# Kernel tuning notes

Hardware: AMD Instinct MI355X
Metric: run time of the kernel (lower is better)

The kernel has to match this reference:

```python
import jax, jax.numpy as jnp
import numpy as np

N_ENT = 50000
N_REL2 = 100   # num_relations * 2
N_BASES = 16
DIM = 64
N_EDGES = 100000


def _rgcn_conv(x, edge_index, edge_type, edge_norm, basis, att, root, bias):
    # x: [N, D]; basis: [B, D, D]; att: [R, B]; root: [D, D]; bias: [D]
    src = edge_index[0]
    dst = edge_index[1]
    num_nodes = x.shape[0]
    # Per-edge relation weight is w[edge_type] with w = att @ basis (reshaped).
    # By linearity we contract x_j with each basis first, then mix with the
    # per-edge attention coefficients -- same math, avoids the [E, D, D] gather.
    coeff = att[edge_type]                          # [E, B]
    xb = jnp.einsum('ei,bio->ebo', x[src], basis)   # [E, B, D]
    msg = jnp.einsum('eb,ebo->eo', coeff, xb)       # [E, D]
    msg = msg * edge_norm[:, None]
    # scatter-mean aggregation at target nodes
    s = jax.ops.segment_sum(msg, dst, num_segments=num_nodes)
    cnt = jax.ops.segment_sum(jnp.ones((msg.shape[0],), msg.dtype), dst,
                              num_segments=num_nodes)
    agg = s / jnp.maximum(cnt, 1.0)[:, None]
    # root transform + bias
    return agg + x @ root + bias


def setup_inputs() -> dict:
    key = jax.random.key(0)
    ks = jax.random.split(key, 12)
    E = N_EDGES
    inp = {
        'entity': jnp.arange(N_ENT, dtype=jnp.int64) if jax.config.jax_enable_x64 else jnp.arange(N_ENT, dtype=jnp.int32),
        'edge_index': jax.random.randint(ks[0], (2, E), 0, N_ENT),
        'edge_type': jax.random.randint(ks[1], (E,), 0, N_REL2),
        'edge_norm': jax.random.uniform(ks[2], (E,), dtype=jnp.float32),
        'emb': jax.random.normal(ks[3], (N_ENT, DIM), dtype=jnp.float32) * 0.1,
        'basis1': jax.random.normal(ks[4], (N_BASES, DIM, DIM), dtype=jnp.float32) * 0.05,
        'att1': jax.random.normal(ks[5], (N_REL2, N_BASES), dtype=jnp.float32) * 0.1,
        'root1': jax.random.normal(ks[6], (DIM, DIM), dtype=jnp.float32) * 0.05,
        'bias1': jnp.zeros((DIM,), dtype=jnp.float32),
        'basis2': jax.random.normal(ks[7], (N_BASES, DIM, DIM), dtype=jnp.float32) * 0.05,
        'att2': jax.random.normal(ks[8], (N_REL2, N_BASES), dtype=jnp.float32) * 0.1,
        'root2': jax.random.normal(ks[9], (DIM, DIM), dtype=jnp.float32) * 0.05,
        'bias2': jnp.zeros((DIM,), dtype=jnp.float32),
    }
    return inp


def reference(entity, edge_index, edge_type, edge_norm, emb,
              basis1, att1, root1, bias1, basis2, att2, root2, bias2):
    x = emb[entity]                                  # embedding lookup [N, D]
    x = _rgcn_conv(x, edge_index, edge_type, edge_norm, basis1, att1, root1, bias1)
    x = _rgcn_conv(x, edge_index, edge_type, edge_norm, basis2, att2, root2, bias2)
    return x
```

## Files before the change

kernel.cpp:

```cpp
#include <hip/hip_runtime.h>

#define NN 50000
#define NR 100
#define NB 16
#define D  64
#define NE 100000
#define NE2 (NE + 16 * NR)

#define HB  196
#define EPB 512
#define ZB  196
#define GB  ((NN * 16 + 255) / 256)

#define GROUPS 2
#define EPBK (64 * GROUPS)
#define EGRID ((NE2 + EPBK - 1) / EPBK)

#define NPBK 128
#define NGRID ((NN + NPBK - 1) / NPBK)

typedef float f32x4  __attribute__((ext_vector_type(4)));
typedef short bf16x8 __attribute__((ext_vector_type(8)));
typedef unsigned short u16;

__device__ __forceinline__ short f2bf(float f) {
    unsigned u = __float_as_uint(f);
    return (short)((u + 0x7FFFu + ((u >> 16) & 1u)) >> 16);
}

__device__ __forceinline__ float bf2f(u16 u) {
    return __uint_as_float((unsigned)u << 16);
}

__device__ __forceinline__ bf16x8 pack8(f32x4 a, f32x4 b) {
    bf16x8 t;
    t[0] = f2bf(a.x); t[1] = f2bf(a.y); t[2] = f2bf(a.z); t[3] = f2bf(a.w);
    t[4] = f2bf(b.x); t[5] = f2bf(b.y); t[6] = f2bf(b.z); t[7] = f2bf(b.w);
    return t;
}

__global__ __launch_bounds__(256) void prep_all(
    const float* __restrict__ att1, const float* __restrict__ basis1,
    const float* __restrict__ root1,
    const float* __restrict__ att2, const float* __restrict__ basis2,
    const float* __restrict__ root2,
    const int* __restrict__ entity, const f32x4* __restrict__ emb4,
    float* __restrict__ Wt1, float* __restrict__ Wt2,
    float* __restrict__ rT1, float* __restrict__ rT2,
    f32x4* __restrict__ x04, int* __restrict__ deg, int* __restrict__ nodeCur)
{
    __shared__ float t[64 * 65];
    int b = blockIdx.x;
    if (b < 2 * NR) {
        int layer = b >= NR;
        int r = layer ? b - NR : b;
        const float* att   = layer ? att2 : att1;
        const float* basis = layer ? basis2 : basis1;
        float*       Wt    = layer ? Wt2 : Wt1;
        float a[NB];
#pragma unroll
        for (int bb = 0; bb < NB; ++bb) a[bb] = att[r * NB + bb];
#pragma unroll
        for (int i = 0; i < 16; ++i) {
            int idx = i * 256 + threadIdx.x;
            float acc = 0.f;
#pragma unroll
            for (int bb = 0; bb < NB; ++bb) acc += a[bb] * basis[bb * 4096 + idx];
            t[(idx >> 6) * 65 + (idx & 63)] = acc;
        }
        __syncthreads();
#pragma unroll
        for (int i = 0; i < 16; ++i) {
            int j = i * 256 + threadIdx.x;
            Wt[(size_t)r * 4096 + j] = t[(j & 63) * 65 + (j >> 6)];
        }
    } else if (b < 2 * NR + 2) {
        const float* root = (b == 2 * NR) ? root1 : root2;
        float*       rT   = (b == 2 * NR) ? rT1 : rT2;
#pragma unroll
        for (int i = 0; i < 16; ++i) {
            int idx = i * 256 + threadIdx.x;
            t[(idx >> 6) * 65 + (idx & 63)] = root[idx];
        }
        __syncthreads();
#pragma unroll
        for (int i = 0; i < 16; ++i) {
            int j = i * 256 + threadIdx.x;
            rT[j] = t[(j & 63) * 65 + (j >> 6)];
        }
    } else if (b < 2 * NR + 2 + ZB) {
        int i = (b - (2 * NR + 2)) * 256 + threadIdx.x;
        deg[i] = 0; nodeCur[i] = 0;
    } else {
        int idx = (b - (2 * NR + 2 + ZB)) * 256 + threadIdx.x;
        if (idx < NN * 16) {
            int n = idx >> 4;
            int q = idx & 15;
            x04[idx] = emb4[(size_t)entity[n] * 16 + q];
        }
    }
}

__global__ __launch_bounds__(256) void hist_edges(
    const int* __restrict__ et, const int* __restrict__ dst,
    int* __restrict__ blockHist, int* __restrict__ deg)
{
    __shared__ int lh[NR];
    for (int i = threadIdx.x; i < NR; i += 256) lh[i] = 0;
    __syncthreads();
#pragma unroll
    for (int i = 0; i < EPB / 256; ++i) {
        int e = blockIdx.x * EPB + i * 256 + threadIdx.x;
        if (e < NE) {
            atomicAdd(&lh[et[e]], 1);
            atomicAdd(&deg[dst[e]], 1);
        }
    }
    __syncthreads();
    for (int i = threadIdx.x; i < NR; i += 256)
        blockHist[blockIdx.x * NR + i] = lh[i];
}

__global__ __launch_bounds__(256) void scans(
    const int* __restrict__ blockHist, int* __restrict__ blockPrefix,
    int* __restrict__ relTot, const int* __restrict__ deg,
    int* __restrict__ nodePre, int* __restrict__ blockSumN)
{
    __shared__ int sc[256];
    int t = threadIdx.x;
    if (blockIdx.x < NR) {
        int r = blockIdx.x;
        int v = (t < HB) ? blockHist[t * NR + r] : 0;
        sc[t] = v;
        __syncthreads();
#pragma unroll
        for (int off = 1; off < 256; off <<= 1) {
            int a = (t >= off) ? sc[t - off] : 0;
            __syncthreads();
            sc[t] += a;
            __syncthreads();
        }
        if (t < HB) blockPrefix[t * NR + r] = sc[t] - v;
        if (t == 0) relTot[r] = sc[255];
    } else {
        int b = blockIdx.x - NR;
        int n = b * 256 + t;
        int v = deg[n];
        sc[t] = v;
        __syncthreads();
#pragma unroll
        for (int off = 1; off < 256; off <<= 1) {
            int a = (t >= off) ? sc[t - off] : 0;
            __syncthreads();
            sc[t] += a;
            __syncthreads();
        }
        nodePre[n] = sc[t] - v;
        if (t == 255) blockSumN[b] = sc[255];
    }
}

__global__ __launch_bounds__(256) void scanK(
    const int* __restrict__ relTot, const int* __restrict__ blockSumN,
    int* __restrict__ offs, int* __restrict__ nbG, int* __restrict__ nodeBB,
    int* __restrict__ srcS, float* __restrict__ normS, int* __restrict__ rS)
{
    __shared__ int totL[NR];
    __shared__ int offL[NR + 1];
    __shared__ int sc2[256];
    int t = threadIdx.x;
    if (t < NR) totL[t] = relTot[t];
    int v2 = (t < ZB) ? blockSumN[t] : 0;
    sc2[t] = v2;
    __syncthreads();
    if (t == 0) {
        int off = 0;
        for (int r = 0; r < NR; ++r) {
            offL[r] = off;
            off = (off + totL[r] + 15) & ~15;
        }
        offL[NR] = off;
    }
    __syncthreads();
#pragma unroll
    for (int off = 1; off < 256; off <<= 1) {
        int a = (t >= off) ? sc2[t - off] : 0;
        __syncthreads();
        sc2[t] += a;
        __syncthreads();
    }
    if (t < ZB) nodeBB[t] = sc2[t] - v2;
    if (t == 0) nodeBB[ZB] = sc2[255];
    if (t <= NR) offs[t] = offL[t];
    if (t == 0) nbG[0] = offL[NR];
    if (t < NR) {
        int g0 = offL[t] + totL[t], g1 = offL[t + 1];
        for (int p = g0; p < g1; ++p) { srcS[p] = 0; normS[p] = 0.f; rS[p] = t; }
    }
}

__global__ __launch_bounds__(256) void scatter2(
    const int* __restrict__ src, const int* __restrict__ dst,
    const int* __restrict__ et, const float* __restrict__ en,
    const int* __restrict__ offs, const int* __restrict__ blockPrefix,
    const int* __restrict__ nodePre, const int* __restrict__ nodeBlockBase,
    int* __restrict__ nodeCur, int* __restrict__ srcS,
    float* __restrict__ normS, int* __restrict__ rS, int* __restrict__ dstIdx)
{
    __shared__ int lcur[NR];
    for (int i = threadIdx.x; i < NR; i += 256)
        lcur[i] = offs[i] + blockPrefix[blockIdx.x * NR + i];
    __syncthreads();
#pragma unroll
    for (int i = 0; i < EPB / 256; ++i) {
        int e = blockIdx.x * EPB + i * 256 + threadIdx.x;
        if (e < NE) {
            int r = et[e];
            int p = atomicAdd(&lcur[r], 1);
            srcS[p] = src[e]; normS[p] = en[e]; rS[p] = r;
            int n = dst[e];
            int q = nodeBlockBase[n >> 8] + nodePre[n] + atomicAdd(&nodeCur[n], 1);
            dstIdx[q] = p;
        }
    }
}

__global__ __launch_bounds__(256) void edge_mfma(
    const int* __restrict__ srcS, const float* __restrict__ normS,
    const int* __restrict__ rS, const int* __restrict__ nbG,
    const float* __restrict__ x, const float* __restrict__ Wt,
    u16* __restrict__ msg)
{
    int tid = threadIdx.x;
    int lane = tid & 63, wid = tid >> 6;
    int c15 = lane & 15, kg = lane >> 4;
    int padTot = nbG[0];
    int rcur = -1;
    bf16x8 B[4][2];

#pragma unroll 1
    for (int g = 0; g < GROUPS; ++g) {
        int gs = blockIdx.x * EPBK + wid * (16 * GROUPS) + g * 16;
        if (gs >= padTot) break;
        int r = __builtin_amdgcn_readfirstlane(rS[gs]);
        if (r != rcur) {
            rcur = r;
            const float* __restrict__ Wr = Wt + (size_t)r * 4096;
#pragma unroll
            for (int nt = 0; nt < 4; ++nt)
#pragma unroll
                for (int ks = 0; ks < 2; ++ks) {
                    const f32x4* p = (const f32x4*)(Wr + (nt * 16 + c15) * 64 + ks * 32 + kg * 8);
                    B[nt][ks] = pack8(p[0], p[1]);
                }
        }
        int e  = gs + c15;
        float nrm = normS[e];
        int   sn  = srcS[e];
        const f32x4* xr  = (const f32x4*)(x + (size_t)sn * 64 + kg * 8);
        const f32x4* xr2 = (const f32x4*)(x + (size_t)sn * 64 + 32 + kg * 8);
        bf16x8 A0 = pack8(xr[0]  * nrm, xr[1]  * nrm);
        bf16x8 A1 = pack8(xr2[0] * nrm, xr2[1] * nrm);

        f32x4 z = {0.f, 0.f, 0.f, 0.f};
        f32x4 acc[4] = {z, z, z, z};
#pragma unroll
        for (int nt = 0; nt < 4; ++nt) {
            acc[nt] = __builtin_amdgcn_mfma_f32_16x16x32_bf16(A0, B[nt][0], acc[nt], 0, 0, 0);
            acc[nt] = __builtin_amdgcn_mfma_f32_16x16x32_bf16(A1, B[nt][1], acc[nt], 0, 0, 0);
        }
#pragma unroll
        for (int nt = 0; nt < 4; ++nt)
#pragma unroll
            for (int j = 0; j < 4; ++j)
                msg[(size_t)(gs + kg * 4 + j) * 64 + nt * 16 + c15] =
                    (u16)f2bf(acc[nt][j]);
    }
}

__global__ __launch_bounds__(256) void agg_mean(
    const u16* __restrict__ msg, const int* __restrict__ dstIdx,
    const int* __restrict__ nodePre, const int* __restrict__ nodeBB,
    float* __restrict__ agg)
{
    int n    = blockIdx.x * 4 + (threadIdx.x >> 6);
    int lane = threadIdx.x & 63;
    if (n >= NN) return;
    int blk  = n >> 8;
    int base = nodeBB[blk];
    int lo = base + nodePre[n];
    int hi = ((n & 255) == 255) ? nodeBB[blk + 1] : base + nodePre[n + 1];
    float acc = 0.f;
    for (int q = lo; q < hi; ++q)
        acc += bf2f(msg[(size_t)dstIdx[q] * 64 + lane]);
    float c = (float)(hi - lo);
    c = c > 1.f ? c : 1.f;
    agg[(size_t)n * 64 + lane] = acc / c;
}

__global__ __launch_bounds__(256) void node_mfma(
    const float* __restrict__ x, const float* __restrict__ agg,
    const float* __restrict__ rT, const float* __restrict__ bias,
    float* __restrict__ out)
{
    int tid = threadIdx.x;
    int lane = tid & 63, wid = tid >> 6;
    int c15 = lane & 15, kg = lane >> 4;

    bf16x8 B[4][2];
#pragma unroll
    for (int nt = 0; nt < 4; ++nt)
#pragma unroll
        for (int ks = 0; ks < 2; ++ks) {
            const f32x4* p = (const f32x4*)(rT + (nt * 16 + c15) * 64 + ks * 32 + kg * 8);
            B[nt][ks] = pack8(p[0], p[1]);
        }
    float bv[4];
#pragma unroll
    for (int nt = 0; nt < 4; ++nt) bv[nt] = bias[nt * 16 + c15];

#pragma unroll 1
    for (int g = 0; g < 2; ++g) {
        int gs = blockIdx.x * NPBK + wid * 32 + g * 16;
        if (gs >= NN) break;
        int ge = gs + 16 < NN ? gs + 16 : NN;

        int n  = gs + c15;
        int nc = n < ge ? n : ge - 1;
        const f32x4* xr  = (const f32x4*)(x + (size_t)nc * 64 + kg * 8);
        const f32x4* xr2 = (const f32x4*)(x + (size_t)nc * 64 + 32 + kg * 8);
        bf16x8 A0 = pack8(xr[0], xr[1]);
        bf16x8 A1 = pack8(xr2[0], xr2[1]);

        f32x4 z = {0.f, 0.f, 0.f, 0.f};
        f32x4 acc[4] = {z, z, z, z};
#pragma unroll
        for (int nt = 0; nt < 4; ++nt) {
            acc[nt] = __builtin_amdgcn_mfma_f32_16x16x32_bf16(A0, B[nt][0], acc[nt], 0, 0, 0);
            acc[nt] = __builtin_amdgcn_mfma_f32_16x16x32_bf16(A1, B[nt][1], acc[nt], 0, 0, 0);
        }
#pragma unroll
        for (int nt = 0; nt < 4; ++nt)
#pragma unroll
            for (int j = 0; j < 4; ++j) {
                int nr = gs + kg * 4 + j;
                if (nr < ge) {
                    size_t off = (size_t)nr * 64 + nt * 16 + c15;
                    out[off] = agg[off] + acc[nt][j] + bv[nt];
                }
            }
    }
}

extern "C" void kernel_launch(void* const* d_in, const int* in_sizes, int n_in,
                              void* d_out, int out_size, void* d_ws, size_t ws_size,
                              hipStream_t stream) {
    const int*   entity    = (const int*)d_in[0];
    const int*   edge_index= (const int*)d_in[1];
    const int*   edge_type = (const int*)d_in[2];
    const float* edge_norm = (const float*)d_in[3];
    const float* emb       = (const float*)d_in[4];
    const float* basis1    = (const float*)d_in[5];
    const float* att1      = (const float*)d_in[6];
    const float* root1     = (const float*)d_in[7];
    const float* bias1     = (const float*)d_in[8];
    const float* basis2    = (const float*)d_in[9];
    const float* att2      = (const float*)d_in[10];
    const float* root2     = (const float*)d_in[11];
    const float* bias2     = (const float*)d_in[12];

    const int* src = edge_index;
    const int* dst = edge_index + NE;

    float* ws    = (float*)d_ws;
    float* Wt1   = ws;
    float* Wt2   = Wt1 + (size_t)NR * 4096;
    float* rT1   = Wt2 + (size_t)NR * 4096;
    float* rT2   = rT1 + 4096;
    float* x0    = rT2 + 4096;
    float* agg   = x0  + (size_t)NN * D;
    float* normS = agg + (size_t)NN * D;
    u16*   msg   = (u16*)(normS + NE2);
    int*   offs        = (int*)(msg + (size_t)NE2 * D);
    int*   relTot      = offs + NR + 3;
    int*   nbG         = relTot + NR;
    int*   blockHist   = nbG + 3;
    int*   blockPrefix = blockHist + HB * NR;
    int*   srcS        = blockPrefix + HB * NR;
    int*   rS          = srcS + NE2;
    int*   deg         = rS + NE2;
    int*   nodePre     = deg + ZB * 256;
    int*   nodeCur     = nodePre + ZB * 256;
    int*   blockSumN   = nodeCur + ZB * 256;
    int*   nodeBB      = blockSumN + ZB + 4;
    int*   dstIdx      = nodeBB + ZB + 5;

    float* out = (float*)d_out;

    prep_all<<<2 * NR + 2 + ZB + GB, 256, 0, stream>>>(
        att1, basis1, root1, att2, basis2, root2,
        entity, (const f32x4*)emb, Wt1, Wt2, rT1, rT2,
        (f32x4*)x0, deg, nodeCur);
    hist_edges<<<HB, 256, 0, stream>>>(edge_type, dst, blockHist, deg);
    scans<<<NR + ZB, 256, 0, stream>>>(blockHist, blockPrefix, relTot,
                                       deg, nodePre, blockSumN);
    scanK<<<1, 256, 0, stream>>>(relTot, blockSumN, offs, nbG, nodeBB,
                                 srcS, normS, rS);
    scatter2<<<HB, 256, 0, stream>>>(src, dst, edge_type, edge_norm,
                                     offs, blockPrefix, nodePre, nodeBB,
                                     nodeCur, srcS, normS, rS, dstIdx);

    edge_mfma<<<EGRID, 256, 0, stream>>>(srcS, normS, rS, nbG, x0, Wt1, msg);
    agg_mean<<<(NN + 3) / 4, 256, 0, stream>>>(msg, dstIdx, nodePre, nodeBB, agg);
    node_mfma<<<NGRID, 256, 0, stream>>>(x0, agg, rT1, bias1, out);

    edge_mfma<<<EGRID, 256, 0, stream>>>(srcS, normS, rS, nbG, out, Wt2, msg);
    agg_mean<<<(NN + 3) / 4, 256, 0, stream>>>(msg, dstIdx, nodePre, nodeBB, agg);
    node_mfma<<<NGRID, 256, 0, stream>>>(out, agg, rT2, bias2, out);
}
```

Before: 136.7 us.

## Store edge messages in fp32 and aggregate four nodes per wave

Edge messages are now stored as fp32 instead of bf16, which removes the rounding step on write and the conversion on read but doubles the message buffer traffic. The aggregation kernel now handles four destination nodes per wave and interleaves their gather loops, so more independent loads are in flight to hide latency. The cost is extra memory bandwidth for writing and reading messages, plus divergence when the four nodes have different degrees.

Result: no change. 139.3 us (+1.8%).

```diff
diff --git a/kernel.cpp b/kernel.cpp
--- a/kernel.cpp
+++ b/kernel.cpp
@@ -19,17 +19,14 @@
 #define NPBK 128
 #define NGRID ((NN + NPBK - 1) / NPBK)
 
+#define AGRID ((NN + 15) / 16)
+
 typedef float f32x4  __attribute__((ext_vector_type(4)));
 typedef short bf16x8 __attribute__((ext_vector_type(8)));
-typedef unsigned short u16;
 
 __device__ __forceinline__ short f2bf(float f) {
     unsigned u = __float_as_uint(f);
     return (short)((u + 0x7FFFu + ((u >> 16) & 1u)) >> 16);
-}
-
-__device__ __forceinline__ float bf2f(u16 u) {
-    return __uint_as_float((unsigned)u << 16);
 }
 
 __device__ __forceinline__ bf16x8 pack8(f32x4 a, f32x4 b) {
@@ -229,7 +226,7 @@
     const int* __restrict__ srcS, const float* __restrict__ normS,
     const int* __restrict__ rS, const int* __restrict__ nbG,
     const float* __restrict__ x, const float* __restrict__ Wt,
-    u16* __restrict__ msg)
+    float* __restrict__ msg)
 {
     int tid = threadIdx.x;
     int lane = tid & 63, wid = tid >> 6;
@@ -273,29 +270,51 @@
         for (int nt = 0; nt < 4; ++nt)
 #pragma unroll
             for (int j = 0; j < 4; ++j)
-                msg[(size_t)(gs + kg * 4 + j) * 64 + nt * 16 + c15] =
-                    (u16)f2bf(acc[nt][j]);
+                msg[(size_t)(gs + kg * 4 + j) * 64 + nt * 16 + c15] = acc[nt][j];
     }
 }
 
 __global__ __launch_bounds__(256) void agg_mean(
-    const u16* __restrict__ msg, const int* __restrict__ dstIdx,
+    const float* __restrict__ msg, const int* __restrict__ dstIdx,
     const int* __restrict__ nodePre, const int* __restrict__ nodeBB,
     float* __restrict__ agg)
 {
-    int n    = blockIdx.x * 4 + (threadIdx.x >> 6);
+    int wave = blockIdx.x * 4 + (threadIdx.x >> 6);
     int lane = threadIdx.x & 63;
-    if (n >= NN) return;
-    int blk  = n >> 8;
-    int base = nodeBB[blk];
-    int lo = base + nodePre[n];
-    int hi = ((n & 255) == 255) ? nodeBB[blk + 1] : base + nodePre[n + 1];
-    float acc = 0.f;
-    for (int q = lo; q < hi; ++q)
-        acc += bf2f(msg[(size_t)dstIdx[q] * 64 + lane]);
-    float c = (float)(hi - lo);
-    c = c > 1.f ? c : 1.f;
-    agg[(size_t)n * 64 + lane] = acc / c;
+    int n0 = wave * 4;
+    if (n0 >= NN) return;
+
+    int lo[4], hi[4];
+#pragma unroll
+    for (int j = 0; j < 4; ++j) {
+        int n = n0 + j;
+        int blk  = n >> 8;
+        int base = nodeBB[blk];
+        lo[j] = base + nodePre[n];
+        hi[j] = ((n & 255) == 255) ? nodeBB[blk + 1] : base + nodePre[n + 1];
+    }
+    int d0 = hi[0] - lo[0], d1 = hi[1] - lo[1];
+    int d2 = hi[2] - lo[2], d3 = hi[3] - lo[3];
+    int maxd = d0 > d1 ? d0 : d1;
+    if (d2 > maxd) maxd = d2;
+    if (d3 > maxd) maxd = d3;
+
+    float acc[4] = {0.f, 0.f, 0.f, 0.f};
+#pragma unroll 1
+    for (int t = 0; t < maxd; ++t) {
+#pragma unroll
+        for (int j = 0; j < 4; ++j) {
+            int q = lo[j] + t;
+            if (q < hi[j])
+                acc[j] += msg[(size_t)dstIdx[q] * 64 + lane];
+        }
+    }
+#pragma unroll
+    for (int j = 0; j < 4; ++j) {
+        float c = (float)(hi[j] - lo[j]);
+        c = c > 1.f ? c : 1.f;
+        agg[(size_t)(n0 + j) * 64 + lane] = acc[j] / c;
+    }
 }
 
 __global__ __launch_bounds__(256) void node_mfma(
@@ -378,10 +397,10 @@
     float* rT1   = Wt2 + (size_t)NR * 4096;
     float* rT2   = rT1 + 4096;
     float* x0    = rT2 + 4096;
-    float* agg   = x0  + (size_t)NN * D;
+    float* msg   = x0  + (size_t)NN * D;
+    float* agg   = msg + (size_t)NE2 * D;
     float* normS = agg + (size_t)NN * D;
-    u16*   msg   = (u16*)(normS + NE2);
-    int*   offs        = (int*)(msg + (size_t)NE2 * D);
+    int*   offs        = (int*)(normS + NE2);
     int*   relTot      = offs + NR + 3;
     int*   nbG         = relTot + NR;
     int*   blockHist   = nbG + 3;
@@ -411,10 +430,10 @@
                                      nodeCur, srcS, normS, rS, dstIdx);
 
     edge_mfma<<<EGRID, 256, 0, stream>>>(srcS, normS, rS, nbG, x0, Wt1, msg);
-    agg_mean<<<(NN + 3) / 4, 256, 0, stream>>>(msg, dstIdx, nodePre, nodeBB, agg);
+    agg_mean<<<AGRID, 256, 0, stream>>>(msg, dstIdx, nodePre, nodeBB, agg);
     node_mfma<<<NGRID, 256, 0, stream>>>(x0, agg, rT1, bias1, out);
 
     edge_mfma<<<EGRID, 256, 0, stream>>>(srcS, normS, rS, nbG, out, Wt2, msg);
-    agg_mean<<<(NN + 3) / 4, 256, 0, stream>>>(msg, dstIdx, nodePre, nodeBB, agg);
+    agg_mean<<<AGRID, 256, 0, stream>>>(msg, dstIdx, nodePre, nodeBB, agg);
     node_mfma<<<NGRID, 256, 0, stream>>>(out, agg, rT2, bias2, out);
 }
```
